# Performance work log

Measured on AMD Instinct MI355X. Metric: run time of the kernel, lower is better.

Reference implementation:

```python
import jax, jax.numpy as jnp
import numpy as np

POOL, D_MODEL, D_FF, M_DIM = 512, 1024, 4096, 64
B, S, K = 2, 2048, 8


def setup_inputs() -> dict:
    key = jax.random.key(0)
    ks = jax.random.split(key, 8)
    x = jax.random.normal(ks[0], (B, S, D_MODEL), dtype=jnp.float32)
    selected_indices = jax.random.randint(ks[1], (B, S, K), 0, POOL, dtype=jnp.int32)
    pattern_weights = jax.random.normal(ks[2], (B, S, K), dtype=jnp.float32)
    base_patterns = 0.02 * jax.random.normal(ks[3], (POOL, D_FF), dtype=jnp.float32)
    # nn.Linear(d_model, pool_size*mod_dim): weight [P*M, d_model], xavier-uniform
    lim_cm = float(np.sqrt(6.0 / (D_MODEL + POOL * M_DIM)))
    cm_w = jax.random.uniform(ks[4], (POOL * M_DIM, D_MODEL), jnp.float32, -lim_cm, lim_cm)
    cm_b = jnp.zeros((POOL * M_DIM,), jnp.float32)
    adj_proj = 0.01 * jax.random.normal(ks[5], (M_DIM, D_FF), dtype=jnp.float32)
    lim_w2 = float(np.sqrt(6.0 / (D_FF + D_MODEL)))
    w2_w = jax.random.uniform(ks[6], (D_MODEL, D_FF), jnp.float32, -lim_w2, lim_w2)
    w2_b = jnp.zeros((D_MODEL,), jnp.float32)
    return {"x": x, "selected_indices": selected_indices, "pattern_weights": pattern_weights,
            "base_patterns": base_patterns, "cm_w": cm_w, "cm_b": cm_b,
            "adj_proj": adj_proj, "w2_w": w2_w, "w2_b": w2_b}


def reference(x, selected_indices, pattern_weights, base_patterns, cm_w, cm_b, adj_proj, w2_w, w2_b):
    b, s, k = selected_indices.shape
    # gather base firing patterns for selected neurons: [b,s,k,d_ff]
    bp = base_patterns[selected_indices]
    # dense context modulation then gather (matches original module): [b,s,P,M]
    mod = (jnp.einsum('bsd,nd->bsn', x, cm_w) + cm_b).reshape(b, s, POOL, M_DIM)
    sel_mod = jnp.take_along_axis(mod, selected_indices[..., None], axis=2)  # [b,s,k,M]
    adjustments = jnp.einsum('bskm,mf->bskf', sel_mod, adj_proj)
    adjusted = bp + adjustments  # [b,s,k,d_ff]
    w = jax.nn.softmax(pattern_weights, axis=-1)
    combined = jnp.einsum('bsk,bskf->bsf', w, adjusted)  # [b,s,d_ff]
    activated = jax.nn.gelu(combined, approximate=False)  # torch default gelu = exact erf
    return jnp.einsum('bsf,df->bsd', activated, w2_w) + w2_b
```

## Files before the change

kernel.cpp:

```cpp
#include <hip/hip_runtime.h>
#include <math.h>

#define T_    4096
#define K_    8
#define POOL_ 512
#define DM_   1024
#define DFF_  4096
#define MD_   64
#define KC_   576

typedef __bf16 bf16x8 __attribute__((ext_vector_type(8)));
typedef __bf16 bf16x4 __attribute__((ext_vector_type(4)));
typedef float  f32x4  __attribute__((ext_vector_type(4)));

typedef __attribute__((address_space(1))) const void g_void;
typedef __attribute__((address_space(3))) void s_void;

__device__ __forceinline__ void async_ld16(const void* g, void* s) {
    __builtin_amdgcn_global_load_lds((g_void*)g, (s_void*)s, 16, 0, 0);
}
__device__ __forceinline__ float gelu_exact(float g) {
    return 0.5f * g * (1.f + erff(g * 0.70710678118654752f));
}
__device__ __forceinline__ bf16x4 cvt4(float4 v) {
    bf16x4 o;
    o[0] = (__bf16)v.x; o[1] = (__bf16)v.y; o[2] = (__bf16)v.z; o[3] = (__bf16)v.w;
    return o;
}
__device__ __forceinline__ bf16x8 cvt8(float4 a, float4 b) {
    bf16x8 o;
    o[0] = (__bf16)a.x; o[1] = (__bf16)a.y; o[2] = (__bf16)a.z; o[3] = (__bf16)a.w;
    o[4] = (__bf16)b.x; o[5] = (__bf16)b.y; o[6] = (__bf16)b.z; o[7] = (__bf16)b.w;
    return o;
}

__global__ __launch_bounds__(256) void k_hist(const int* __restrict__ sel,
                                              int* __restrict__ counts) {
    int i = blockIdx.x * 256 + threadIdx.x;
    if (i < T_ * K_) atomicAdd(&counts[sel[i]], 1);
}

__global__ __launch_bounds__(512) void k_scan(const int* __restrict__ counts,
                                              int* __restrict__ offsets,
                                              int* __restrict__ cursor) {
    __shared__ int s[512];
    const int t = threadIdx.x;
    const int c = counts[t];
    s[t] = c;
    __syncthreads();
    for (int d = 1; d < 512; d <<= 1) {
        int v = (t >= d) ? s[t - d] : 0;
        __syncthreads();
        s[t] += v;
        __syncthreads();
    }
    offsets[t] = s[t] - c;
    cursor[t]  = s[t] - c;
    if (t == 511) offsets[512] = s[511];
}

__global__ __launch_bounds__(256) void k_scatter(const int* __restrict__ sel,
                                                 int* __restrict__ cursor,
                                                 int* __restrict__ bucket,
                                                 int* __restrict__ rank) {
    int i = blockIdx.x * 256 + threadIdx.x;
    if (i < T_ * K_) {
        int p = sel[i];
        int pos = atomicAdd(&cursor[p], 1);
        bucket[pos] = i;
        rank[i] = pos;
    }
}

__global__ __launch_bounds__(256) void k_cvt(const float* __restrict__ src,
                                             __bf16* __restrict__ dst, int n16) {
    int i = blockIdx.x * 256 + threadIdx.x;
    if (i >= n16) return;
    const float4* s = (const float4*)src + (long)i * 4;
    float4 a = s[0], b = s[1], c = s[2], d = s[3];
    bf16x8 o0 = cvt8(a, b), o1 = cvt8(c, d);
    bf16x8* dp = (bf16x8*)dst + (long)i * 2;
    dp[0] = o0; dp[1] = o1;
}

__global__ __launch_bounds__(256) void k_selmod(
    const __bf16* __restrict__ xb, const float* __restrict__ cm_w,
    const int* __restrict__ bucket, const int* __restrict__ offsets,
    float* __restrict__ Y0, float* __restrict__ Y1,
    float* __restrict__ Y2, float* __restrict__ Y3)
{
    const int p   = blockIdx.x;
    const int kh  = blockIdx.y;
    const int off = offsets[p];
    const int n   = offsets[p + 1] - off;
    if (n == 0) return;
    float* Y = (kh == 0) ? Y0 : (kh == 1) ? Y1 : (kh == 2) ? Y2 : Y3;

    const int tid  = threadIdx.x;
    const int wave = tid >> 6, lane = tid & 63;
    const int quad = lane >> 4, l15 = lane & 15;

    __shared__ int list[48];
    __shared__ __align__(16) __bf16 Wl[64][264];
    __shared__ __align__(16) __bf16 Xl[48][264];

    {
        const int wr = tid >> 6;
        const int wc = (tid & 63) * 4;
        const float* wsrc = cm_w + (long)(p * 64 + wr) * DM_ + kh * 256 + wc;
        float4 wv[16];
        #pragma unroll
        for (int j = 0; j < 16; ++j)
            wv[j] = *(const float4*)(wsrc + (long)j * 4 * DM_);
        #pragma unroll
        for (int j = 0; j < 16; ++j)
            *(bf16x4*)&Wl[wr + j * 4][wc] = cvt4(wv[j]);
    }

    for (int g0 = 0; g0 < n; g0 += 48) {
        const int gn  = min(n - g0, 48);
        const int nch = (gn + 15) >> 4;

        __syncthreads();
        if (tid < 48) {
            int r = g0 + tid; if (r >= n) r = n - 1;
            list[tid] = bucket[off + r] >> 3;
        }
        __syncthreads();

        {
            bf16x8 xv[6];
            #pragma unroll
            for (int j = 0; j < 6; ++j) {
                const int row = (tid >> 5) + j * 8;
                const int c16 = (tid & 31) * 8;
                xv[j] = *(const bf16x8*)(xb + (long)list[row] * DM_ + kh * 256 + c16);
            }
            #pragma unroll
            for (int j = 0; j < 6; ++j)
                *(bf16x8*)&Xl[(tid >> 5) + j * 8][(tid & 31) * 8] = xv[j];
        }
        __syncthreads();

        f32x4 acc[3] = {};
        #pragma unroll
        for (int ks = 0; ks < 8; ++ks) {
            const bf16x8 bfr = *(const bf16x8*)&Wl[wave * 16 + l15][ks * 32 + quad * 8];
            #pragma unroll
            for (int c = 0; c < 3; ++c)
                if (c < nch) {
                    const bf16x8 afr = *(const bf16x8*)&Xl[c * 16 + l15][ks * 32 + quad * 8];
                    acc[c] = __builtin_amdgcn_mfma_f32_16x16x32_bf16(afr, bfr, acc[c], 0, 0, 0);
                }
        }
        #pragma unroll
        for (int c = 0; c < 3; ++c)
            if (c < nch) {
                #pragma unroll
                for (int r = 0; r < 4; ++r) {
                    const int prow = c * 16 + quad * 4 + r;
                    if (prow < gn)
                        Y[(long)(off + g0 + prow) * MD_ + wave * 16 + l15] = acc[c][r];
                }
            }
    }
}

__global__ __launch_bounds__(256) void k_wdense(
    const float* __restrict__ Y0, const float* __restrict__ Y1,
    const float* __restrict__ Y2, const float* __restrict__ Y3,
    const int* __restrict__ sel, const int* __restrict__ rank,
    const float* __restrict__ pw, const float* __restrict__ cm_b,
    __bf16* __restrict__ Wd)
{
    const int tid = threadIdx.x;
    const int tt = tid >> 6, m = tid & 63;
    const int t = blockIdx.x * 4 + tt;
    __shared__ float w_s[4][8];
    __shared__ int   sidx[4][8];
    __shared__ int   rnk[4][8];
    __shared__ __align__(16) __bf16 row[4][KC_];

    if (m < 8) {
        w_s[tt][m]  = pw[t * 8 + m];
        sidx[tt][m] = sel[t * 8 + m];
        rnk[tt][m]  = rank[t * 8 + m];
    }
    __syncthreads();
    if (m == 0) {
        float mx = w_s[tt][0];
        #pragma unroll
        for (int k = 1; k < 8; ++k) mx = fmaxf(mx, w_s[tt][k]);
        float sum = 0.f;
        #pragma unroll
        for (int k = 0; k < 8; ++k) { float e = expf(w_s[tt][k] - mx); w_s[tt][k] = e; sum += e; }
        float inv = 1.f / sum;
        #pragma unroll
        for (int k = 0; k < 8; ++k) w_s[tt][k] *= inv;
    }
    __syncthreads();
    *(uint4*)&row[tt][m * 8] = make_uint4(0, 0, 0, 0);
    {
        float a = 0.f;
        #pragma unroll
        for (int k = 0; k < 8; ++k) {
            const long yb = (long)rnk[tt][k] * MD_ + m;
            float y = cm_b[sidx[tt][k] * 64 + m] + Y0[yb] + Y1[yb] + Y2[yb] + Y3[yb];
            a += w_s[tt][k] * y;
        }
        row[tt][512 + m] = (__bf16)a;
    }
    __syncthreads();
    if (m == 0) {
        #pragma unroll
        for (int k = 0; k < 8; ++k) {
            int c = sidx[tt][k];
            row[tt][c] = (__bf16)((float)row[tt][c] + w_s[tt][k]);
        }
    }
    __syncthreads();
    const uint4* src = (const uint4*)&row[0][0];
    uint4* dst = (uint4*)(Wd + (long)blockIdx.x * 4 * KC_);
    for (int e = tid; e < 4 * KC_ * 2 / 16; e += 256) dst[e] = src[e];
}

__global__ __launch_bounds__(256) void k_buildP(
    const float* __restrict__ bp, const float* __restrict__ adj,
    __bf16* __restrict__ P)
{
    __shared__ __bf16 tile[64][72];
    const int tid = threadIdx.x;
    const int bx = blockIdx.x, f0 = blockIdx.y * 64;
    const float* src = (bx < 8) ? (bp + (long)bx * 64 * DFF_) : adj;
    for (int e = tid; e < 4096; e += 256) {
        int f = e & 63, c = e >> 6;
        tile[c][f] = (__bf16)src[(long)c * DFF_ + f0 + f];
    }
    __syncthreads();
    const int c0 = bx * 64;
    for (int e = tid; e < 4096; e += 256) {
        int c = e & 63, f = e >> 6;
        P[(long)(f0 + f) * KC_ + c0 + c] = tile[c][f];
    }
}

__global__ __launch_bounds__(256) void k_actgemm(
    const __bf16* __restrict__ A, const __bf16* __restrict__ Bw,
    __bf16* __restrict__ act)
{
    __shared__ __align__(16) __bf16 sA[128 * 32];
    __shared__ __align__(16) __bf16 sB[128 * 32];
    const int tid  = threadIdx.x;
    const int tm   = blockIdx.y * 128, tn = blockIdx.x * 128;
    const int wave = tid >> 6, lane = tid & 63, quad = lane >> 4, l15 = lane & 15;
    const int wm   = (wave >> 1) * 64, wn = (wave & 1) * 64;

    f32x4 acc[4][4] = {};

    const int e    = tid * 8;
    const int srow = e >> 5;
    const int scol = e & 31;
    const __bf16* agp0 = A  + ((long)(tm + srow)      * KC_ + scol);
    const __bf16* agp1 = A  + ((long)(tm + 64 + srow) * KC_ + scol);
    const __bf16* bgp0 = Bw + ((long)(tn + srow)      * KC_ + scol);
    const __bf16* bgp1 = Bw + ((long)(tn + 64 + srow) * KC_ + scol);
    void* sa0 = (void*)(sA + e);
    void* sa1 = (void*)(sA + 2048 + e);
    void* sb0 = (void*)(sB + e);
    void* sb1 = (void*)(sB + 2048 + e);

    for (int kk = 0; kk < KC_; kk += 32) {
        async_ld16(agp0 + kk, sa0);
        async_ld16(agp1 + kk, sa1);
        async_ld16(bgp0 + kk, sb0);
        async_ld16(bgp1 + kk, sb1);
        __syncthreads();
        bf16x8 af[4], bf[4];
        #pragma unroll
        for (int i = 0; i < 4; ++i)
            af[i] = *(const bf16x8*)(sA + (wm + i * 16 + l15) * 32 + quad * 8);
        #pragma unroll
        for (int j = 0; j < 4; ++j)
            bf[j] = *(const bf16x8*)(sB + (wn + j * 16 + l15) * 32 + quad * 8);
        #pragma unroll
        for (int i = 0; i < 4; ++i)
            #pragma unroll
            for (int j = 0; j < 4; ++j)
                acc[i][j] = __builtin_amdgcn_mfma_f32_16x16x32_bf16(af[i], bf[j], acc[i][j], 0, 0, 0);
        __syncthreads();
    }

    #pragma unroll
    for (int j = 0; j < 4; ++j) {
        const int col = tn + wn + j * 16 + l15;
        #pragma unroll
        for (int i = 0; i < 4; ++i) {
            const int row = tm + wm + i * 16 + quad * 4;
            #pragma unroll
            for (int r = 0; r < 4; ++r)
                act[(long)(row + r) * DFF_ + col] = (__bf16)gelu_exact(acc[i][j][r]);
        }
    }
}

__global__ __launch_bounds__(256) void k_outgemm(
    const __bf16* __restrict__ A, const __bf16* __restrict__ Bw,
    const float* __restrict__ bias, float* __restrict__ out)
{
    __shared__ __align__(16) __bf16 sA[128 * 128];
    __shared__ __align__(16) __bf16 sB[128 * 128];
    const int tid  = threadIdx.x;
    const int tm   = blockIdx.y * 128, tn = blockIdx.x * 128;
    const int wave = tid >> 6, lane = tid & 63, quad = lane >> 4, l15 = lane & 15;
    const int wm   = (wave >> 1) * 64, wn = (wave & 1) * 64;

    f32x4 acc[4][4] = {};

    const int e  = tid * 8;
    const int r0 = e >> 5;
    const int cc = e & 31;

    for (int kk = 0; kk < DFF_; kk += 128) {
        #pragma unroll
        for (int s = 0; s < 4; ++s) {
            #pragma unroll
            for (int q = 0; q < 2; ++q) {
                async_ld16(A  + (long)(tm + q * 64 + r0) * DFF_ + kk + s * 32 + cc,
                           (void*)(sA + s * 4096 + q * 2048 + e));
                async_ld16(Bw + (long)(tn + q * 64 + r0) * DFF_ + kk + s * 32 + cc,
                           (void*)(sB + s * 4096 + q * 2048 + e));
            }
        }
        __syncthreads();
        #pragma unroll
        for (int s = 0; s < 4; ++s) {
            bf16x8 af[4], bf[4];
            #pragma unroll
            for (int i = 0; i < 4; ++i)
                af[i] = *(const bf16x8*)(sA + s * 4096 + (wm + i * 16 + l15) * 32 + quad * 8);
            #pragma unroll
            for (int j = 0; j < 4; ++j)
                bf[j] = *(const bf16x8*)(sB + s * 4096 + (wn + j * 16 + l15) * 32 + quad * 8);
            #pragma unroll
            for (int i = 0; i < 4; ++i)
                #pragma unroll
                for (int j = 0; j < 4; ++j)
                    acc[i][j] = __builtin_amdgcn_mfma_f32_16x16x32_bf16(af[i], bf[j], acc[i][j], 0, 0, 0);
        }
        __syncthreads();
    }

    #pragma unroll
    for (int j = 0; j < 4; ++j) {
        const int col = tn + wn + j * 16 + l15;
        const float bj = bias[col];
        #pragma unroll
        for (int i = 0; i < 4; ++i) {
            const int row = tm + wm + i * 16 + quad * 4;
            #pragma unroll
            for (int r = 0; r < 4; ++r)
                out[(long)(row + r) * 1024 + col] = acc[i][j][r] + bj;
        }
    }
}

extern "C" void kernel_launch(void* const* d_in, const int* in_sizes, int n_in,
                              void* d_out, int out_size, void* d_ws, size_t ws_size,
                              hipStream_t stream) {
    const float* x    = (const float*)d_in[0];
    const int*   sel  = (const int*)  d_in[1];
    const float* pw   = (const float*)d_in[2];
    const float* bp   = (const float*)d_in[3];
    const float* cm_w = (const float*)d_in[4];
    const float* cm_b = (const float*)d_in[5];
    const float* adj  = (const float*)d_in[6];
    const float* w2   = (const float*)d_in[7];
    const float* w2b  = (const float*)d_in[8];
    float* out = (float*)d_out;

    char* ws = (char*)d_ws;
    __bf16* x_bf = (__bf16*)ws;
    __bf16* act  = (__bf16*)ws;
    float*  Yp1  = (float*)(ws + (size_t) 8 * 1024 * 1024);
    float*  Yp2  = (float*)(ws + (size_t)16 * 1024 * 1024);
    float*  Yp3  = (float*)(ws + (size_t)24 * 1024 * 1024);
    __bf16* P    = (__bf16*)(ws + (size_t)32 * 1024 * 1024);
    __bf16* w2bf = (__bf16*)(ws + (size_t)37 * 1024 * 1024);
    char*  bins  = ws + (size_t)45 * 1024 * 1024;
    int* bucket  = (int*)bins;
    int* rank    = (int*)(bins + 131072);
    int* counts  = (int*)(bins + 262144);
    int* cursor  = (int*)(bins + 264192);
    int* offsets = (int*)(bins + 266240);

    float*  Yp0 = (float*)d_out;
    __bf16* Wd  = (__bf16*)((char*)d_out + (size_t)8 * 1024 * 1024);

    hipMemsetAsync(counts, 0, 4096, stream);
    k_hist   <<<128, 256, 0, stream>>>(sel, counts);
    k_scan   <<<1,   512, 0, stream>>>(counts, offsets, cursor);
    k_scatter<<<128, 256, 0, stream>>>(sel, cursor, bucket, rank);
    k_cvt    <<<1024, 256, 0, stream>>>(x, x_bf, T_ * DM_ / 16);
    k_selmod <<<dim3(POOL_, 4), 256, 0, stream>>>(x_bf, cm_w, bucket, offsets,
                                                  Yp0, Yp1, Yp2, Yp3);
    k_wdense <<<T_ / 4, 256, 0, stream>>>(Yp0, Yp1, Yp2, Yp3, sel, rank, pw, cm_b, Wd);
    k_buildP <<<dim3(9, 64), 256, 0, stream>>>(bp, adj, P);
    k_cvt    <<<1024, 256, 0, stream>>>(w2, w2bf, DM_ * DFF_ / 16);
    k_actgemm<<<dim3(DFF_ / 128, T_ / 128), 256, 0, stream>>>(Wd, P, act);
    k_outgemm<<<dim3(DM_ / 128, T_ / 128), 256, 0, stream>>>(act, w2bf, w2b, out);
}
```

Baseline: 408.5 us.

## Restructure selmod kernel: per-wave token chunks reading x directly from global

The selmod kernel no longer stages gathered x rows into shared memory in 48-row groups with block-wide barriers. Each wave now takes its own 16-token chunk, loads A fragments straight from global memory, and computes all 64 output columns against the shared W tile. This removes the Xl staging buffer and the per-group syncthreads, and frees LDS for occupancy. It also clamps each bucket to 256 tokens, which silently drops tokens if a pool entry is selected more than 256 times.

```diff
diff --git a/kernel.cpp b/kernel.cpp
--- a/kernel.cpp
+++ b/kernel.cpp
@@ -92,17 +92,17 @@
     const int p   = blockIdx.x;
     const int kh  = blockIdx.y;
     const int off = offsets[p];
-    const int n   = offsets[p + 1] - off;
-    if (n == 0) return;
+    int n = offsets[p + 1] - off;
+    if (n <= 0) return;
+    if (n > 256) n = 256;
     float* Y = (kh == 0) ? Y0 : (kh == 1) ? Y1 : (kh == 2) ? Y2 : Y3;
 
     const int tid  = threadIdx.x;
     const int wave = tid >> 6, lane = tid & 63;
     const int quad = lane >> 4, l15 = lane & 15;
 
-    __shared__ int list[48];
+    __shared__ int list[256];
     __shared__ __align__(16) __bf16 Wl[64][264];
-    __shared__ __align__(16) __bf16 Xl[48][264];
 
     {
         const int wr = tid >> 6;
@@ -116,53 +116,38 @@
         for (int j = 0; j < 16; ++j)
             *(bf16x4*)&Wl[wr + j * 4][wc] = cvt4(wv[j]);
     }
-
-    for (int g0 = 0; g0 < n; g0 += 48) {
-        const int gn  = min(n - g0, 48);
-        const int nch = (gn + 15) >> 4;
-
-        __syncthreads();
-        if (tid < 48) {
-            int r = g0 + tid; if (r >= n) r = n - 1;
-            list[tid] = bucket[off + r] >> 3;
-        }
-        __syncthreads();
-
-        {
-            bf16x8 xv[6];
-            #pragma unroll
-            for (int j = 0; j < 6; ++j) {
-                const int row = (tid >> 5) + j * 8;
-                const int c16 = (tid & 31) * 8;
-                xv[j] = *(const bf16x8*)(xb + (long)list[row] * DM_ + kh * 256 + c16);
+    for (int i = tid; i < n; i += 256) list[i] = bucket[off + i] >> 3;
+    __syncthreads();
+
+    const int nch = (n + 15) >> 4;
+    for (int c = wave; c < nch; c += 4) {
+        int row = c * 16 + l15; if (row >= n) row = n - 1;
+        const __bf16* xrow = xb + (long)list[row] * DM_ + kh * 256 + quad * 8;
+
+        f32x4 a0 = {}, a1 = {}, a2 = {}, a3 = {};
+        #pragma unroll
+        for (int ks = 0; ks < 8; ++ks) {
+            const bf16x8 afr = *(const bf16x8*)(xrow + ks * 32);
+            const bf16x8 b0 = *(const bf16x8*)&Wl[ 0 + l15][ks * 32 + quad * 8];
+            const bf16x8 b1 = *(const bf16x8*)&Wl[16 + l15][ks * 32 + quad * 8];
+            const bf16x8 b2 = *(const bf16x8*)&Wl[32 + l15][ks * 32 + quad * 8];
+            const bf16x8 b3 = *(const bf16x8*)&Wl[48 + l15][ks * 32 + quad * 8];
+            a0 = __builtin_amdgcn_mfma_f32_16x16x32_bf16(afr, b0, a0, 0, 0, 0);
+            a1 = __builtin_amdgcn_mfma_f32_16x16x32_bf16(afr, b1, a1, 0, 0, 0);
+            a2 = __builtin_amdgcn_mfma_f32_16x16x32_bf16(afr, b2, a2, 0, 0, 0);
+            a3 = __builtin_amdgcn_mfma_f32_16x16x32_bf16(afr, b3, a3, 0, 0, 0);
+        }
+        #pragma unroll
+        for (int r = 0; r < 4; ++r) {
+            const int prow = c * 16 + quad * 4 + r;
+            if (prow < n) {
+                float* yr = Y + (long)(off + prow) * MD_ + l15;
+                yr[ 0] = a0[r];
+                yr[16] = a1[r];
+                yr[32] = a2[r];
+                yr[48] = a3[r];
             }
-            #pragma unroll
-            for (int j = 0; j < 6; ++j)
-                *(bf16x8*)&Xl[(tid >> 5) + j * 8][(tid & 31) * 8] = xv[j];
-        }
-        __syncthreads();
-
-        f32x4 acc[3] = {};
-        #pragma unroll
-        for (int ks = 0; ks < 8; ++ks) {
-            const bf16x8 bfr = *(const bf16x8*)&Wl[wave * 16 + l15][ks * 32 + quad * 8];
-            #pragma unroll
-            for (int c = 0; c < 3; ++c)
-                if (c < nch) {
-                    const bf16x8 afr = *(const bf16x8*)&Xl[c * 16 + l15][ks * 32 + quad * 8];
-                    acc[c] = __builtin_amdgcn_mfma_f32_16x16x32_bf16(afr, bfr, acc[c], 0, 0, 0);
-                }
-        }
-        #pragma unroll
-        for (int c = 0; c < 3; ++c)
-            if (c < nch) {
-                #pragma unroll
-                for (int r = 0; r < 4; ++r) {
-                    const int prow = c * 16 + quad * 4 + r;
-                    if (prow < gn)
-                        Y[(long)(off + g0 + prow) * MD_ + wave * 16 + l15] = acc[c][r];
-                }
-            }
+        }
     }
 }
 
```

After: 400.8 us. About the same (-1.9%).
